# Kernel tuning notes

Measured on AMD Instinct MI355X. Metric: run time of the kernel, lower is better.

## Reference

```python
import jax, jax.numpy as jnp
import numpy as np
import math

B, S = 8, 2048
N_HIDDEN_RNN = 512
D_MODEL = 1024
NUM_HEADS = 16
N_OUTPUT = 1024
SCALE = math.sqrt(D_MODEL // NUM_HEADS)  # head_dim used only for scaling


def setup_inputs() -> dict:
    key = jax.random.key(0)
    ks = jax.random.split(key, 11)
    def lin(k, fan_in, fan_out):
        bound = 1.0 / math.sqrt(fan_in)
        kw, kb = jax.random.split(k)
        W = jax.random.uniform(kw, (fan_out, fan_in), jnp.float32, -bound, bound)
        b = jax.random.uniform(kb, (fan_out,), jnp.float32, -bound, bound)
        return W, b
    Wq, bq = lin(ks[0], N_HIDDEN_RNN, D_MODEL)
    Wk, bk = lin(ks[1], D_MODEL, D_MODEL)
    Wv, bv = lin(ks[2], D_MODEL, D_MODEL)
    Wo, bo = lin(ks[3], D_MODEL, N_OUTPUT)
    return {
        "query": jax.random.normal(ks[4], (B, S, N_HIDDEN_RNN), jnp.float32),
        "key": jax.random.normal(ks[5], (B, S, D_MODEL), jnp.float32),
        "value": jax.random.normal(ks[6], (B, S, D_MODEL), jnp.float32),
        "Wq": Wq, "bq": bq, "Wk": Wk, "bk": bk,
        "Wv": Wv, "bv": bv, "Wo": Wo, "bo": bo,
    }


def reference(query, key, value, Wq, bq, Wk, bk, Wv, bv, Wo, bo):
    # Projections
    q = query @ Wq.T + bq      # [B, S, d_model]
    k = key @ Wk.T + bk        # [B, S, d_model]
    v = value @ Wv.T + bv      # [B, S, d_model]
    # Original code transposes to [B, d_model, S] (feature-axis attention).
    # scores[b, i, j] = sum_s q[b, s, i] * k[b, s, j] / scale -> [B, d, d]
    scores = jnp.einsum('bsi,bsj->bij', q, k) / SCALE
    probs = jax.nn.softmax(scores, axis=-1)   # softmax over feature axis j
    # out[b, s, i] = sum_j probs[b, i, j] * v[b, s, j]
    attn_out = jnp.einsum('bij,bsj->bsi', probs, v)  # [B, S, d_model]
    return attn_out @ Wo.T + bo  # [B, S, n_output]
```

## Files before the change

### kernel.cpp

```cpp
#include <hip/hip_runtime.h>
#include <hip/hip_bf16.h>
#include <stdint.h>

typedef __bf16 b16x8 __attribute__((ext_vector_type(8)));
typedef float  f32x4 __attribute__((ext_vector_type(4)));

__device__ __forceinline__ unsigned short f2bf(float f) {
    uint32_t u = __float_as_uint(f);
    u += 0x7fffu + ((u >> 16) & 1u);
    return (unsigned short)(u >> 16);
}
__device__ __forceinline__ float bf2f(unsigned short s) {
    return __uint_as_float(((uint32_t)s) << 16);
}

__device__ __forceinline__ void gld16(const unsigned short* g, unsigned short* l) {
    __builtin_amdgcn_global_load_lds(
        (const __attribute__((address_space(1))) void*)g,
        (__attribute__((address_space(3))) void*)l, 16, 0, 0);
}

__global__ void k_detect(const unsigned short* __restrict__ q, int n, int* __restrict__ flag) {
    float m = 0.f;
    for (int i = threadIdx.x; i < n; i += 256) {
        float f = fabsf(bf2f(q[i]));
        if (!(f < 1e30f)) f = 1e30f;
        m = fmaxf(m, f);
    }
#pragma unroll
    for (int o = 32; o > 0; o >>= 1) m = fmaxf(m, __shfl_xor(m, o));
    __shared__ float red[4];
    if ((threadIdx.x & 63) == 0) red[threadIdx.x >> 6] = m;
    __syncthreads();
    if (threadIdx.x == 0) {
        m = fmaxf(fmaxf(red[0], red[1]), fmaxf(red[2], red[3]));
        flag[0] = (m > 1e6f) ? 1 : 0;
    }
}

__global__ __launch_bounds__(256) void k_cvt(const void* __restrict__ src,
                                             unsigned short* __restrict__ dst,
                                             long n8, const int* __restrict__ flag) {
    long i = blockIdx.x * 256L + threadIdx.x;
    long stride = (long)gridDim.x * 256L;
    if (flag[0]) {
        const float4* s = (const float4*)src;
        for (long j = i; j < n8; j += stride) {
            float4 a = s[2 * j], b = s[2 * j + 1];
            uint4 o;
            o.x = f2bf(a.x) | ((uint32_t)f2bf(a.y) << 16);
            o.y = f2bf(a.z) | ((uint32_t)f2bf(a.w) << 16);
            o.z = f2bf(b.x) | ((uint32_t)f2bf(b.y) << 16);
            o.w = f2bf(b.z) | ((uint32_t)f2bf(b.w) << 16);
            ((uint4*)dst)[j] = o;
        }
    } else {
        const uint4* s = (const uint4*)src;
        for (long j = i; j < n8; j += stride) ((uint4*)dst)[j] = s[j];
    }
}

__global__ __launch_bounds__(256) void k_cvt_bias(const void* b0, const void* b1,
                                                  const void* b2, const void* b3,
                                                  float* __restrict__ dst,
                                                  const int* __restrict__ flag) {
    int i = blockIdx.x * 256 + threadIdx.x;
    int which = i >> 10, idx = i & 1023;
    const void* src = (which == 0) ? b0 : (which == 1) ? b1 : (which == 2) ? b2 : b3;
    dst[i] = flag[0] ? ((const float*)src)[idx] : bf2f(((const unsigned short*)src)[idx]);
}

template <int MODE>
__global__ __launch_bounds__(512, 2) void k_gemm2(
    const unsigned short* __restrict__ A, const unsigned short* __restrict__ B,
    const float* __restrict__ bias, void* __restrict__ Cv,
    int N, int K, int ldA, int ldB, int lb,
    long sAb, long sBb, long sCb, float scale,
    const int* __restrict__ flagp)
{
    extern __shared__ unsigned short lds_raw[];
    const int tid  = threadIdx.x;
    const int lane = tid & 63;
    const int wave = tid >> 6;
    const int bn = blockIdx.x * 256;
    const int bm = blockIdx.y * 256;
    const int batch = bm >> lb;
    const int am0 = bm & ((1 << lb) - 1);
    const int Mb = 1 << lb;
    const unsigned short* Ab = A + (long)batch * sAb;
    const unsigned short* Bb = B + (long)batch * sBb;
    const long zC = (long)batch * sCb;
    const int wm = (wave >> 2) * 128;
    const int wn = (wave & 3) * 64;

    f32x4 acc[8][4];
    const f32x4 zero = {0.f, 0.f, 0.f, 0.f};
#pragma unroll
    for (int i = 0; i < 8; ++i)
#pragma unroll
        for (int j = 0; j < 4; ++j) acc[i][j] = zero;

    auto stage = [&](int kt, int cb) {
        unsigned short* LA = lds_raw + (size_t)cb * 32768;
        unsigned short* LB = LA + 16384;
#pragma unroll
        for (int j = 0; j < 4; ++j) {
            const int d = j * 512 + tid;
            const int row = d >> 3;
            const int klo = (d & 7) ^ (row & 7);
            gld16(Ab + (long)(am0 + row) * ldA + kt * 64 + klo * 8, LA + (size_t)d * 8);
            gld16(Bb + (long)(bn + row) * ldB + kt * 64 + klo * 8, LB + (size_t)d * 8);
        }
    };

    auto ctile = [&](int cb) {
        const unsigned short* LA = lds_raw + (size_t)cb * 32768;
        const unsigned short* LB = LA + 16384;
        b16x8 bfr[4][2];
#pragma unroll
        for (int p = 0; p < 4; ++p) {
            if (p == 0) {
#pragma unroll
                for (int j = 0; j < 4; ++j)
#pragma unroll
                    for (int s = 0; s < 2; ++s) {
                        const int r = wn + j * 16 + (lane & 15);
                        const int kl = s * 4 + (lane >> 4);
                        bfr[j][s] = *(const b16x8*)(LB + ((size_t)r * 8 + (kl ^ (r & 7))) * 8);
                    }
            }
            b16x8 a[2][2];
#pragma unroll
            for (int q = 0; q < 2; ++q)
#pragma unroll
                for (int s = 0; s < 2; ++s) {
                    const int r = wm + (2 * p + q) * 16 + (lane & 15);
                    const int kl = s * 4 + (lane >> 4);
                    a[q][s] = *(const b16x8*)(LA + ((size_t)r * 8 + (kl ^ (r & 7))) * 8);
                }
            __builtin_amdgcn_s_setprio(1);
#pragma unroll
            for (int q = 0; q < 2; ++q)
#pragma unroll
                for (int j = 0; j < 4; ++j)
#pragma unroll
                    for (int s = 0; s < 2; ++s)
                        acc[2 * p + q][j] = __builtin_amdgcn_mfma_f32_16x16x32_bf16(
                            a[q][s], bfr[j][s], acc[2 * p + q][j], 0, 0, 0);
            __builtin_amdgcn_s_setprio(0);
        }
    };

    const int NT = K >> 6;
    stage(0, 0);
    __syncthreads();
    int cur = 0;
    for (int kt = 0; kt < NT - 1; ++kt) {
        stage(kt + 1, cur ^ 1);
        ctile(cur);
        __syncthreads();
        cur ^= 1;
    }
    ctile(cur);

    const int fl = flagp ? flagp[0] : 1;
#pragma unroll
    for (int i = 0; i < 8; ++i)
#pragma unroll
        for (int j = 0; j < 4; ++j) {
            const int rloc = am0 + wm + i * 16 + (lane >> 4) * 4;
            const int n    = bn + wn + j * 16 + (lane & 15);
            const float bv = (MODE != 2 && bias != nullptr) ? bias[n] : 0.f;
            if (MODE == 0) {
                unsigned short* C = (unsigned short*)Cv;
#pragma unroll
                for (int r = 0; r < 4; ++r)
                    C[zC + (long)(rloc + r) * N + n] = f2bf(acc[i][j][r] * scale + bv);
            } else if (MODE == 1) {
                unsigned short* C = (unsigned short*)Cv;
                uint32_t p0 = f2bf(acc[i][j][0] * scale + bv) |
                              ((uint32_t)f2bf(acc[i][j][1] * scale + bv) << 16);
                uint32_t p1 = f2bf(acc[i][j][2] * scale + bv) |
                              ((uint32_t)f2bf(acc[i][j][3] * scale + bv) << 16);
                uint2 val; val.x = p0; val.y = p1;
                *(uint2*)(C + zC + (long)n * Mb + rloc) = val;
            } else if (MODE == 2) {
                float* C = (float*)Cv;
#pragma unroll
                for (int r = 0; r < 4; ++r)
                    C[zC + (long)(rloc + r) * N + n] = acc[i][j][r] * scale;
            } else {
                if (fl) {
                    float* C = (float*)Cv;
#pragma unroll
                    for (int r = 0; r < 4; ++r)
                        C[zC + (long)(rloc + r) * N + n] = acc[i][j][r] * scale + bv;
                } else {
                    unsigned short* C = (unsigned short*)Cv;
#pragma unroll
                    for (int r = 0; r < 4; ++r)
                        C[zC + (long)(rloc + r) * N + n] = f2bf(acc[i][j][r] * scale + bv);
                }
            }
        }
}

__global__ __launch_bounds__(256) void k_softmax(float* __restrict__ S) {
    const long row = blockIdx.x;
    float* s = S + row * 1024;
    unsigned short* p = (unsigned short*)s;
    const int tid = threadIdx.x;
    float4 v = ((const float4*)s)[tid];
    float m = fmaxf(fmaxf(v.x, v.y), fmaxf(v.z, v.w));
#pragma unroll
    for (int o = 32; o > 0; o >>= 1) m = fmaxf(m, __shfl_xor(m, o));
    __shared__ float sm[4], ss[4];
    if ((tid & 63) == 0) sm[tid >> 6] = m;
    __syncthreads();
    m = fmaxf(fmaxf(sm[0], sm[1]), fmaxf(sm[2], sm[3]));
    float e0 = __expf(v.x - m), e1 = __expf(v.y - m);
    float e2 = __expf(v.z - m), e3 = __expf(v.w - m);
    float sum = e0 + e1 + e2 + e3;
#pragma unroll
    for (int o = 32; o > 0; o >>= 1) sum += __shfl_xor(sum, o);
    if ((tid & 63) == 0) ss[tid >> 6] = sum;
    __syncthreads();
    float inv = 1.f / (ss[0] + ss[1] + ss[2] + ss[3]);
    uint32_t w0 = f2bf(e0 * inv) | ((uint32_t)f2bf(e1 * inv) << 16);
    uint32_t w1 = f2bf(e2 * inv) | ((uint32_t)f2bf(e3 * inv) << 16);
    uint2 val; val.x = w0; val.y = w1;
    *(uint2*)(p + tid * 4) = val;
}

extern "C" void kernel_launch(void* const* d_in, const int* in_sizes, int n_in,
                              void* d_out, int out_size, void* d_ws, size_t ws_size,
                              hipStream_t stream) {
    (void)in_sizes; (void)n_in; (void)out_size; (void)ws_size;
    const void* q_in = d_in[0];
    const void* k_in = d_in[1];
    const void* v_in = d_in[2];
    const void* Wq   = d_in[3];
    const void* bq   = d_in[4];
    const void* Wk   = d_in[5];
    const void* bk   = d_in[6];
    const void* Wv   = d_in[7];
    const void* bv   = d_in[8];
    const void* Wo   = d_in[9];
    const void* bo   = d_in[10];

    const size_t MB = 1u << 20;
    const size_t LDSB = 131072;
    hipFuncSetAttribute((const void*)k_gemm2<0>, hipFuncAttributeMaxDynamicSharedMemorySize, (int)LDSB);
    hipFuncSetAttribute((const void*)k_gemm2<1>, hipFuncAttributeMaxDynamicSharedMemorySize, (int)LDSB);
    hipFuncSetAttribute((const void*)k_gemm2<2>, hipFuncAttributeMaxDynamicSharedMemorySize, (int)LDSB);
    hipFuncSetAttribute((const void*)k_gemm2<3>, hipFuncAttributeMaxDynamicSharedMemorySize, (int)LDSB);

    char* ws = (char*)d_ws;
    int*            flag = (int*)ws;
    unsigned short* R1   = (unsigned short*)(ws + 1 * MB);
    unsigned short* R2   = (unsigned short*)(ws + 33 * MB);
    char*           R3   = ws + 65 * MB;
    unsigned short* kb = R1, *qb = R1, *vb = R1;
    unsigned short* Kt = R2, *attn = R2;
    float*          scores = (float*)R1;
    unsigned short* P      = R1;
    unsigned short* wqb = (unsigned short*)R3;
    unsigned short* wkb = (unsigned short*)(R3 + 1 * MB);
    unsigned short* wvb = (unsigned short*)(R3 + 3 * MB);
    unsigned short* wob = (unsigned short*)(R3 + 5 * MB);
    float*          bias4 = (float*)(R3 + 7 * MB);
    unsigned short* Vp = (unsigned short*)d_out;
    unsigned short* Qt = (unsigned short*)((char*)d_out + 32 * MB);

    dim3 blk(256);
    k_detect<<<1, blk, 0, stream>>>((const unsigned short*)q_in, 4096, flag);
    k_cvt_bias<<<16, blk, 0, stream>>>(bq, bk, bv, bo, bias4, flag);
    k_cvt<<<256, blk, 0, stream>>>(Wq, wqb, 1024L * 512 / 8, flag);
    k_cvt<<<512, blk, 0, stream>>>(Wk, wkb, 1024L * 1024 / 8, flag);
    k_cvt<<<512, blk, 0, stream>>>(Wv, wvb, 1024L * 1024 / 8, flag);
    k_cvt<<<512, blk, 0, stream>>>(Wo, wob, 1024L * 1024 / 8, flag);

    dim3 blk5(512);
    k_cvt<<<2048, blk, 0, stream>>>(k_in, kb, 8L * 2048 * 1024 / 8, flag);
    k_gemm2<1><<<dim3(4, 64), blk5, LDSB, stream>>>(
        kb, wkb, bias4 + 1024, Kt, 1024, 1024, 1024, 1024, 11,
        2048L * 1024, 0, 1024L * 2048, 1.f, nullptr);
    k_cvt<<<2048, blk, 0, stream>>>(q_in, qb, 8L * 2048 * 512 / 8, flag);
    k_gemm2<1><<<dim3(4, 64), blk5, LDSB, stream>>>(
        qb, wqb, bias4, Qt, 1024, 512, 512, 512, 11,
        2048L * 512, 0, 1024L * 2048, 1.f, nullptr);
    k_cvt<<<2048, blk, 0, stream>>>(v_in, vb, 8L * 2048 * 1024 / 8, flag);
    k_gemm2<0><<<dim3(4, 64), blk5, LDSB, stream>>>(
        vb, wvb, bias4 + 2 * 1024, Vp, 1024, 1024, 1024, 1024, 24,
        0, 0, 0, 1.f, nullptr);
    k_gemm2<2><<<dim3(4, 32), blk5, LDSB, stream>>>(
        Qt, Kt, nullptr, scores, 1024, 2048, 2048, 2048, 10,
        1024L * 2048, 1024L * 2048, 1024L * 1024, 0.125f, nullptr);
    k_softmax<<<dim3(8192), blk, 0, stream>>>(scores);
    k_gemm2<0><<<dim3(4, 64), blk5, LDSB, stream>>>(
        Vp, P, nullptr, attn, 1024, 1024, 1024, 2048, 11,
        2048L * 1024, 1024L * 2048, 2048L * 1024, 1.f, nullptr);
    k_gemm2<3><<<dim3(4, 64), blk5, LDSB, stream>>>(
        attn, wob, bias4 + 3 * 1024, d_out, 1024, 1024, 1024, 1024, 24,
        0, 0, 0, 1.f, flag);
}
```

Measured before the change: 322.0 us.

## Interleave next-tile global loads across MFMA phases with fine-grained waitcnt barriers

Replaces the GEMM main loop with a software pipeline that issues the next K-tile's global-to-LDS loads in four quarters, one per compute phase, guarded by explicit vmcnt waits and s_barriers. This replaces the single bulk stage plus full __syncthreads per tile. Warp row assignment is reshuffled to match the quarter loading order. Block IDs are also remapped so consecutive IDs spread across the eight XCDs. The aim is better overlap of memory with MFMA and better L2 locality, at the cost of hand-tuned waitcnt counts that could race if the compiler reorders loads.

Measured after the change: 319.0 us. About the same (-0.9%).

```diff
diff --git a/kernel.cpp b/kernel.cpp
--- a/kernel.cpp
+++ b/kernel.cpp
@@ -71,7 +71,7 @@
 }
 
 template <int MODE>
-__global__ __launch_bounds__(512, 2) void k_gemm2(
+__global__ __launch_bounds__(512, 2) void k_gemm3(
     const unsigned short* __restrict__ A, const unsigned short* __restrict__ B,
     const float* __restrict__ bias, void* __restrict__ Cv,
     int N, int K, int ldA, int ldB, int lb,
@@ -82,15 +82,19 @@
     const int tid  = threadIdx.x;
     const int lane = tid & 63;
     const int wave = tid >> 6;
-    const int bn = blockIdx.x * 256;
-    const int bm = blockIdx.y * 256;
+    const int nwg = gridDim.x * gridDim.y;
+    const int bid = blockIdx.y * gridDim.x + blockIdx.x;
+    const int nq  = nwg >> 3;
+    const int vb  = (bid & 7) * nq + (bid >> 3);
+    const int bn  = (vb & (gridDim.x - 1)) * 256;
+    const int bm  = (vb / gridDim.x) * 256;
     const int batch = bm >> lb;
     const int am0 = bm & ((1 << lb) - 1);
     const int Mb = 1 << lb;
     const unsigned short* Ab = A + (long)batch * sAb;
     const unsigned short* Bb = B + (long)batch * sBb;
     const long zC = (long)batch * sCb;
-    const int wm = (wave >> 2) * 128;
+    const int g  = wave >> 2;
     const int wn = (wave & 3) * 64;
 
     f32x4 acc[8][4];
@@ -100,25 +104,41 @@
 #pragma unroll
         for (int j = 0; j < 4; ++j) acc[i][j] = zero;
 
-    auto stage = [&](int kt, int cb) {
-        unsigned short* LA = lds_raw + (size_t)cb * 32768;
-        unsigned short* LB = LA + 16384;
-#pragma unroll
-        for (int j = 0; j < 4; ++j) {
-            const int d = j * 512 + tid;
-            const int row = d >> 3;
-            const int klo = (d & 7) ^ (row & 7);
-            gld16(Ab + (long)(am0 + row) * ldA + kt * 64 + klo * 8, LA + (size_t)d * 8);
-            gld16(Bb + (long)(bn + row) * ldB + kt * 64 + klo * 8, LB + (size_t)d * 8);
+    auto stageQ = [&](int kt, int cb, int q) {
+        unsigned short* Lbase = lds_raw + (size_t)cb * 32768 + ((q < 2) ? 16384 : 0);
+#pragma unroll
+        for (int j = 0; j < 2; ++j) {
+            const int c = (q & 1) * 1024 + j * 512 + tid;
+            const int row = c >> 3;
+            const int klo = (c & 7) ^ (row & 7);
+            if (q < 2)
+                gld16(Bb + (long)(bn + row) * ldB + kt * 64 + klo * 8, Lbase + (size_t)c * 8);
+            else
+                gld16(Ab + (long)(am0 + row) * ldA + kt * 64 + klo * 8, Lbase + (size_t)c * 8);
         }
     };
 
-    auto ctile = [&](int cb) {
-        const unsigned short* LA = lds_raw + (size_t)cb * 32768;
+    const int NT = K >> 6;
+#pragma unroll
+    for (int q = 0; q < 4; ++q) stageQ(0, 0, q);
+
+    int cur = 0;
+    for (int t = 0; t < NT; ++t) {
+        const int has_next = (t + 1 < NT);
+        const unsigned short* LA = lds_raw + (size_t)cur * 32768;
         const unsigned short* LB = LA + 16384;
         b16x8 bfr[4][2];
 #pragma unroll
         for (int p = 0; p < 4; ++p) {
+            if (p == 0) {
+                asm volatile("s_waitcnt vmcnt(2)" ::: "memory");
+            } else if (p == 2) {
+                if (has_next) asm volatile("s_waitcnt vmcnt(4)" ::: "memory");
+                else          asm volatile("s_waitcnt vmcnt(0)" ::: "memory");
+            }
+            __builtin_amdgcn_sched_barrier(0);
+            __builtin_amdgcn_s_barrier();
+            asm volatile("" ::: "memory");
             if (p == 0) {
 #pragma unroll
                 for (int j = 0; j < 4; ++j)
@@ -129,53 +149,47 @@
                         bfr[j][s] = *(const b16x8*)(LB + ((size_t)r * 8 + (kl ^ (r & 7))) * 8);
                     }
             }
-            b16x8 a[2][2];
-#pragma unroll
-            for (int q = 0; q < 2; ++q)
+            b16x8 afr[2][2];
+#pragma unroll
+            for (int r = 0; r < 2; ++r)
 #pragma unroll
                 for (int s = 0; s < 2; ++s) {
-                    const int r = wm + (2 * p + q) * 16 + (lane & 15);
+                    const int row = (p >> 1) * 128 + (p & 1) * 64 + g * 32 + r * 16 + (lane & 15);
                     const int kl = s * 4 + (lane >> 4);
-                    a[q][s] = *(const b16x8*)(LA + ((size_t)r * 8 + (kl ^ (r & 7))) * 8);
+                    afr[r][s] = *(const b16x8*)(LA + ((size_t)row * 8 + (kl ^ (row & 7))) * 8);
                 }
+            if (has_next) stageQ(t + 1, cur ^ 1, p);
+            asm volatile("" ::: "memory");
+            __builtin_amdgcn_s_barrier();
+            __builtin_amdgcn_sched_barrier(0);
             __builtin_amdgcn_s_setprio(1);
 #pragma unroll
-            for (int q = 0; q < 2; ++q)
+            for (int r = 0; r < 2; ++r)
 #pragma unroll
                 for (int j = 0; j < 4; ++j)
 #pragma unroll
                     for (int s = 0; s < 2; ++s)
-                        acc[2 * p + q][j] = __builtin_amdgcn_mfma_f32_16x16x32_bf16(
-                            a[q][s], bfr[j][s], acc[2 * p + q][j], 0, 0, 0);
+                        acc[p * 2 + r][j] = __builtin_amdgcn_mfma_f32_16x16x32_bf16(
+                            afr[r][s], bfr[j][s], acc[p * 2 + r][j], 0, 0, 0);
             __builtin_amdgcn_s_setprio(0);
         }
-    };
-
-    const int NT = K >> 6;
-    stage(0, 0);
-    __syncthreads();
-    int cur = 0;
-    for (int kt = 0; kt < NT - 1; ++kt) {
-        stage(kt + 1, cur ^ 1);
-        ctile(cur);
-        __syncthreads();
         cur ^= 1;
     }
-    ctile(cur);
 
     const int fl = flagp ? flagp[0] : 1;
 #pragma unroll
-    for (int i = 0; i < 8; ++i)
+    for (int i = 0; i < 8; ++i) {
+        const int p = i >> 1, r = i & 1;
+        const int rloc = am0 + (p >> 1) * 128 + (p & 1) * 64 + g * 32 + r * 16 + (lane >> 4) * 4;
 #pragma unroll
         for (int j = 0; j < 4; ++j) {
-            const int rloc = am0 + wm + i * 16 + (lane >> 4) * 4;
-            const int n    = bn + wn + j * 16 + (lane & 15);
+            const int n = bn + wn + j * 16 + (lane & 15);
             const float bv = (MODE != 2 && bias != nullptr) ? bias[n] : 0.f;
             if (MODE == 0) {
                 unsigned short* C = (unsigned short*)Cv;
 #pragma unroll
-                for (int r = 0; r < 4; ++r)
-                    C[zC + (long)(rloc + r) * N + n] = f2bf(acc[i][j][r] * scale + bv);
+                for (int rr = 0; rr < 4; ++rr)
+                    C[zC + (long)(rloc + rr) * N + n] = f2bf(acc[i][j][rr] * scale + bv);
             } else if (MODE == 1) {
                 unsigned short* C = (unsigned short*)Cv;
                 uint32_t p0 = f2bf(acc[i][j][0] * scale + bv) |
@@ -187,22 +201,23 @@
             } else if (MODE == 2) {
                 float* C = (float*)Cv;
 #pragma unroll
-                for (int r = 0; r < 4; ++r)
-                    C[zC + (long)(rloc + r) * N + n] = acc[i][j][r] * scale;
+                for (int rr = 0; rr < 4; ++rr)
+                    C[zC + (long)(rloc + rr) * N + n] = acc[i][j][rr] * scale;
             } else {
                 if (fl) {
                     float* C = (float*)Cv;
 #pragma unroll
-                    for (int r = 0; r < 4; ++r)
-                        C[zC + (long)(rloc + r) * N + n] = acc[i][j][r] * scale + bv;
+                    for (int rr = 0; rr < 4; ++rr)
+                        C[zC + (long)(rloc + rr) * N + n] = acc[i][j][rr] * scale + bv;
                 } else {
                     unsigned short* C = (unsigned short*)Cv;
 #pragma unroll
-                    for (int r = 0; r < 4; ++r)
-                        C[zC + (long)(rloc + r) * N + n] = f2bf(acc[i][j][r] * scale + bv);
+                    for (int rr = 0; rr < 4; ++rr)
+                        C[zC + (long)(rloc + rr) * N + n] = f2bf(acc[i][j][rr] * scale + bv);
                 }
             }
         }
+    }
 }
 
 __global__ __launch_bounds__(256) void k_softmax(float* __restrict__ S) {
@@ -250,10 +265,10 @@
 
     const size_t MB = 1u << 20;
     const size_t LDSB = 131072;
-    hipFuncSetAttribute((const void*)k_gemm2<0>, hipFuncAttributeMaxDynamicSharedMemorySize, (int)LDSB);
-    hipFuncSetAttribute((const void*)k_gemm2<1>, hipFuncAttributeMaxDynamicSharedMemorySize, (int)LDSB);
-    hipFuncSetAttribute((const void*)k_gemm2<2>, hipFuncAttributeMaxDynamicSharedMemorySize, (int)LDSB);
-    hipFuncSetAttribute((const void*)k_gemm2<3>, hipFuncAttributeMaxDynamicSharedMemorySize, (int)LDSB);
+    hipFuncSetAttribute((const void*)k_gemm3<0>, hipFuncAttributeMaxDynamicSharedMemorySize, (int)LDSB);
+    hipFuncSetAttribute((const void*)k_gemm3<1>, hipFuncAttributeMaxDynamicSharedMemorySize, (int)LDSB);
+    hipFuncSetAttribute((const void*)k_gemm3<2>, hipFuncAttributeMaxDynamicSharedMemorySize, (int)LDSB);
+    hipFuncSetAttribute((const void*)k_gemm3<3>, hipFuncAttributeMaxDynamicSharedMemorySize, (int)LDSB);
 
     char* ws = (char*)d_ws;
     int*            flag = (int*)ws;
@@ -282,25 +297,25 @@
 
     dim3 blk5(512);
     k_cvt<<<2048, blk, 0, stream>>>(k_in, kb, 8L * 2048 * 1024 / 8, flag);
-    k_gemm2<1><<<dim3(4, 64), blk5, LDSB, stream>>>(
+    k_gemm3<1><<<dim3(4, 64), blk5, LDSB, stream>>>(
         kb, wkb, bias4 + 1024, Kt, 1024, 1024, 1024, 1024, 11,
         2048L * 1024, 0, 1024L * 2048, 1.f, nullptr);
     k_cvt<<<2048, blk, 0, stream>>>(q_in, qb, 8L * 2048 * 512 / 8, flag);
-    k_gemm2<1><<<dim3(4, 64), blk5, LDSB, stream>>>(
+    k_gemm3<1><<<dim3(4, 64), blk5, LDSB, stream>>>(
         qb, wqb, bias4, Qt, 1024, 512, 512, 512, 11,
         2048L * 512, 0, 1024L * 2048, 1.f, nullptr);
     k_cvt<<<2048, blk, 0, stream>>>(v_in, vb, 8L * 2048 * 1024 / 8, flag);
-    k_gemm2<0><<<dim3(4, 64), blk5, LDSB, stream>>>(
+    k_gemm3<0><<<dim3(4, 64), blk5, LDSB, stream>>>(
         vb, wvb, bias4 + 2 * 1024, Vp, 1024, 1024, 1024, 1024, 24,
         0, 0, 0, 1.f, nullptr);
-    k_gemm2<2><<<dim3(4, 32), blk5, LDSB, stream>>>(
+    k_gemm3<2><<<dim3(4, 32), blk5, LDSB, stream>>>(
         Qt, Kt, nullptr, scores, 1024, 2048, 2048, 2048, 10,
         1024L * 2048, 1024L * 2048, 1024L * 1024, 0.125f, nullptr);
     k_softmax<<<dim3(8192), blk, 0, stream>>>(scores);
-    k_gemm2<0><<<dim3(4, 64), blk5, LDSB, stream>>>(
+    k_gemm3<0><<<dim3(4, 64), blk5, LDSB, stream>>>(
         Vp, P, nullptr, attn, 1024, 1024, 1024, 2048, 11,
         2048L * 1024, 1024L * 2048, 2048L * 1024, 1.f, nullptr);
-    k_gemm2<3><<<dim3(4, 64), blk5, LDSB, stream>>>(
+    k_gemm3<3><<<dim3(4, 64), blk5, LDSB, stream>>>(
         attn, wob, bias4 + 3 * 1024, d_out, 1024, 1024, 1024, 1024, 24,
         0, 0, 0, 1.f, flag);
 }
```

## Fuse input fp32-to-bf16 conversion into projection GEMMs and merge setup kernels

Applied to the files above, without the earlier changes.

The projection GEMMs now read fp32 activations directly through registers, convert them to bf16 and write them into swizzled LDS, which removes three standalone conversion passes and their round trips through global memory. The detect, bias and weight conversion kernels are merged into one setup kernel, cutting launch count. Workgroup IDs are also remapped across groups of eight, likely to improve cache locality or XCD distribution. In exchange, the A-operand path moves from async global-to-LDS loads to register staging, which raises register pressure and adds conversion work inside the main loop.

Result: slower. 472.1 us (+46.6%).

```diff
diff --git a/kernel.cpp b/kernel.cpp
--- a/kernel.cpp
+++ b/kernel.cpp
@@ -20,10 +20,17 @@
         (__attribute__((address_space(3))) void*)l, 16, 0, 0);
 }
 
-__global__ void k_detect(const unsigned short* __restrict__ q, int n, int* __restrict__ flag) {
+__global__ __launch_bounds__(256) void k_setup(
+    const unsigned short* __restrict__ qraw,
+    const void* Wq, const void* bq, const void* Wk, const void* bk,
+    const void* Wv, const void* bv, const void* Wo, const void* bo,
+    unsigned short* __restrict__ wqb, unsigned short* __restrict__ wkb,
+    unsigned short* __restrict__ wvb, unsigned short* __restrict__ wob,
+    float* __restrict__ bias4, int* __restrict__ flag)
+{
     float m = 0.f;
-    for (int i = threadIdx.x; i < n; i += 256) {
-        float f = fabsf(bf2f(q[i]));
+    for (int i = threadIdx.x; i < 4096; i += 256) {
+        float f = fabsf(bf2f(qraw[i]));
         if (!(f < 1e30f)) f = 1e30f;
         m = fmaxf(m, f);
     }
@@ -32,47 +39,42 @@
     __shared__ float red[4];
     if ((threadIdx.x & 63) == 0) red[threadIdx.x >> 6] = m;
     __syncthreads();
-    if (threadIdx.x == 0) {
-        m = fmaxf(fmaxf(red[0], red[1]), fmaxf(red[2], red[3]));
-        flag[0] = (m > 1e6f) ? 1 : 0;
+    m = fmaxf(fmaxf(red[0], red[1]), fmaxf(red[2], red[3]));
+    const int fl = (m > 1e6f) ? 1 : 0;
+    if (blockIdx.x == 0 && threadIdx.x == 0) flag[0] = fl;
+
+    if (blockIdx.x < 16) {
+        int i = blockIdx.x * 256 + threadIdx.x;
+        int which = i >> 10, idx = i & 1023;
+        const void* src = (which == 0) ? bq : (which == 1) ? bk : (which == 2) ? bv : bo;
+        bias4[i] = fl ? ((const float*)src)[idx] : bf2f(((const unsigned short*)src)[idx]);
     }
-}
-
-__global__ __launch_bounds__(256) void k_cvt(const void* __restrict__ src,
-                                             unsigned short* __restrict__ dst,
-                                             long n8, const int* __restrict__ flag) {
-    long i = blockIdx.x * 256L + threadIdx.x;
-    long stride = (long)gridDim.x * 256L;
-    if (flag[0]) {
-        const float4* s = (const float4*)src;
-        for (long j = i; j < n8; j += stride) {
-            float4 a = s[2 * j], b = s[2 * j + 1];
+
+    const long NW = 65536L + 3 * 131072L;
+    for (long c = blockIdx.x * 256L + threadIdx.x; c < NW; c += (long)gridDim.x * 256L) {
+        const void* src; unsigned short* dst; long off;
+        if (c < 65536)       { src = Wq; dst = wqb; off = c; }
+        else if (c < 196608) { src = Wk; dst = wkb; off = c - 65536; }
+        else if (c < 327680) { src = Wv; dst = wvb; off = c - 196608; }
+        else                 { src = Wo; dst = wob; off = c - 327680; }
+        if (fl) {
+            const float4* s = (const float4*)src + 2 * off;
+            float4 a = s[0], b = s[1];
             uint4 o;
             o.x = f2bf(a.x) | ((uint32_t)f2bf(a.y) << 16);
             o.y = f2bf(a.z) | ((uint32_t)f2bf(a.w) << 16);
             o.z = f2bf(b.x) | ((uint32_t)f2bf(b.y) << 16);
             o.w = f2bf(b.z) | ((uint32_t)f2bf(b.w) << 16);
-            ((uint4*)dst)[j] = o;
-        }
-    } else {
-        const uint4* s = (const uint4*)src;
-        for (long j = i; j < n8; j += stride) ((uint4*)dst)[j] = s[j];
+            ((uint4*)dst)[off] = o;
+        } else {
+            ((uint4*)dst)[off] = ((const uint4*)src)[off];
+        }
     }
 }
 
-__global__ __launch_bounds__(256) void k_cvt_bias(const void* b0, const void* b1,
-                                                  const void* b2, const void* b3,
-                                                  float* __restrict__ dst,
-                                                  const int* __restrict__ flag) {
-    int i = blockIdx.x * 256 + threadIdx.x;
-    int which = i >> 10, idx = i & 1023;
-    const void* src = (which == 0) ? b0 : (which == 1) ? b1 : (which == 2) ? b2 : b3;
-    dst[i] = flag[0] ? ((const float*)src)[idx] : bf2f(((const unsigned short*)src)[idx]);
-}
-
-template <int MODE>
-__global__ __launch_bounds__(512, 2) void k_gemm2(
-    const unsigned short* __restrict__ A, const unsigned short* __restrict__ B,
+template <int MODE, int AF32>
+__global__ __launch_bounds__(512, 2) void k_gemmU(
+    const void* __restrict__ Araw, const unsigned short* __restrict__ B,
     const float* __restrict__ bias, void* __restrict__ Cv,
     int N, int K, int ldA, int ldB, int lb,
     long sAb, long sBb, long sCb, float scale,
@@ -82,12 +84,16 @@
     const int tid  = threadIdx.x;
     const int lane = tid & 63;
     const int wave = tid >> 6;
-    const int bn = blockIdx.x * 256;
-    const int bm = blockIdx.y * 256;
+    const int nwg = gridDim.x * gridDim.y;
+    const int bid = blockIdx.y * gridDim.x + blockIdx.x;
+    const int vb  = (bid & 7) * (nwg >> 3) + (bid >> 3);
+    const int bn  = (vb & (gridDim.x - 1)) * 256;
+    const int bm  = (vb / gridDim.x) * 256;
     const int batch = bm >> lb;
     const int am0 = bm & ((1 << lb) - 1);
     const int Mb = 1 << lb;
-    const unsigned short* Ab = A + (long)batch * sAb;
+    const int fl = flagp ? flagp[0] : 1;
+    const long aoff = (long)batch * sAb;
     const unsigned short* Bb = B + (long)batch * sBb;
     const long zC = (long)batch * sCb;
     const int wm = (wave >> 2) * 128;
@@ -100,19 +106,64 @@
 #pragma unroll
         for (int j = 0; j < 4; ++j) acc[i][j] = zero;
 
-    auto stage = [&](int kt, int cb) {
+    auto stageB = [&](int kt, int cb) {
+        unsigned short* LB = lds_raw + (size_t)cb * 32768 + 16384;
+#pragma unroll
+        for (int j = 0; j < 4; ++j) {
+            const int d = j * 512 + tid;
+            const int row = d >> 3;
+            const int klo = (d & 7) ^ (row & 7);
+            gld16(Bb + (long)(bn + row) * ldB + kt * 64 + klo * 8, LB + (size_t)d * 8);
+        }
+    };
+    auto stageA = [&](int kt, int cb) {
         unsigned short* LA = lds_raw + (size_t)cb * 32768;
-        unsigned short* LB = LA + 16384;
+        const unsigned short* Ab = (const unsigned short*)Araw + aoff;
 #pragma unroll
         for (int j = 0; j < 4; ++j) {
             const int d = j * 512 + tid;
             const int row = d >> 3;
             const int klo = (d & 7) ^ (row & 7);
             gld16(Ab + (long)(am0 + row) * ldA + kt * 64 + klo * 8, LA + (size_t)d * 8);
-            gld16(Bb + (long)(bn + row) * ldB + kt * 64 + klo * 8, LB + (size_t)d * 8);
-        }
-    };
-
+        }
+    };
+    float4 araw[4][2];
+    uint4  abf[4];
+    auto loadA = [&](int kt) {
+#pragma unroll
+        for (int j = 0; j < 4; ++j) {
+            const int c = j * 512 + tid;
+            const int row = c >> 3, kc = c & 7;
+            if (fl) {
+                const float* s = (const float*)Araw + aoff + (long)(am0 + row) * ldA + kt * 64 + kc * 8;
+                araw[j][0] = *(const float4*)s;
+                araw[j][1] = *(const float4*)(s + 4);
+            } else {
+                abf[j] = *(const uint4*)((const unsigned short*)Araw + aoff +
+                                         (long)(am0 + row) * ldA + kt * 64 + kc * 8);
+            }
+        }
+    };
+    auto cvtWriteA = [&](int cb) {
+        unsigned short* LA = lds_raw + (size_t)cb * 32768;
+#pragma unroll
+        for (int j = 0; j < 4; ++j) {
+            const int c = j * 512 + tid;
+            const int row = c >> 3, kc = c & 7;
+            const int slot = row * 8 + (kc ^ (row & 7));
+            uint4 o;
+            if (fl) {
+                float4 a = araw[j][0], b = araw[j][1];
+                o.x = f2bf(a.x) | ((uint32_t)f2bf(a.y) << 16);
+                o.y = f2bf(a.z) | ((uint32_t)f2bf(a.w) << 16);
+                o.z = f2bf(b.x) | ((uint32_t)f2bf(b.y) << 16);
+                o.w = f2bf(b.z) | ((uint32_t)f2bf(b.w) << 16);
+            } else {
+                o = abf[j];
+            }
+            *(uint4*)(LA + (size_t)slot * 8) = o;
+        }
+    };
     auto ctile = [&](int cb) {
         const unsigned short* LA = lds_raw + (size_t)cb * 32768;
         const unsigned short* LB = LA + 16384;
@@ -152,18 +203,32 @@
     };
 
     const int NT = K >> 6;
-    stage(0, 0);
-    __syncthreads();
     int cur = 0;
-    for (int kt = 0; kt < NT - 1; ++kt) {
-        stage(kt + 1, cur ^ 1);
+    if (AF32) {
+        stageB(0, 0); loadA(0); cvtWriteA(0);
+        __syncthreads();
+        for (int kt = 0; kt < NT - 1; ++kt) {
+            stageB(kt + 1, cur ^ 1);
+            loadA(kt + 1);
+            ctile(cur);
+            cvtWriteA(cur ^ 1);
+            __syncthreads();
+            cur ^= 1;
+        }
         ctile(cur);
+    } else {
+        stageA(0, 0); stageB(0, 0);
         __syncthreads();
-        cur ^= 1;
+        for (int kt = 0; kt < NT - 1; ++kt) {
+            stageA(kt + 1, cur ^ 1);
+            stageB(kt + 1, cur ^ 1);
+            ctile(cur);
+            __syncthreads();
+            cur ^= 1;
+        }
+        ctile(cur);
     }
-    ctile(cur);
-
-    const int fl = flagp ? flagp[0] : 1;
+
 #pragma unroll
     for (int i = 0; i < 8; ++i)
 #pragma unroll
@@ -250,17 +315,17 @@
 
     const size_t MB = 1u << 20;
     const size_t LDSB = 131072;
-    hipFuncSetAttribute((const void*)k_gemm2<0>, hipFuncAttributeMaxDynamicSharedMemorySize, (int)LDSB);
-    hipFuncSetAttribute((const void*)k_gemm2<1>, hipFuncAttributeMaxDynamicSharedMemorySize, (int)LDSB);
-    hipFuncSetAttribute((const void*)k_gemm2<2>, hipFuncAttributeMaxDynamicSharedMemorySize, (int)LDSB);
-    hipFuncSetAttribute((const void*)k_gemm2<3>, hipFuncAttributeMaxDynamicSharedMemorySize, (int)LDSB);
+    hipFuncSetAttribute((const void*)k_gemmU<1, 1>, hipFuncAttributeMaxDynamicSharedMemorySize, (int)LDSB);
+    hipFuncSetAttribute((const void*)k_gemmU<0, 1>, hipFuncAttributeMaxDynamicSharedMemorySize, (int)LDSB);
+    hipFuncSetAttribute((const void*)k_gemmU<2, 0>, hipFuncAttributeMaxDynamicSharedMemorySize, (int)LDSB);
+    hipFuncSetAttribute((const void*)k_gemmU<0, 0>, hipFuncAttributeMaxDynamicSharedMemorySize, (int)LDSB);
+    hipFuncSetAttribute((const void*)k_gemmU<3, 0>, hipFuncAttributeMaxDynamicSharedMemorySize, (int)LDSB);
 
     char* ws = (char*)d_ws;
     int*            flag = (int*)ws;
     unsigned short* R1   = (unsigned short*)(ws + 1 * MB);
     unsigned short* R2   = (unsigned short*)(ws + 33 * MB);
     char*           R3   = ws + 65 * MB;
-    unsigned short* kb = R1, *qb = R1, *vb = R1;
     unsigned short* Kt = R2, *attn = R2;
     float*          scores = (float*)R1;
     unsigned short* P      = R1;
@@ -272,35 +337,28 @@
     unsigned short* Vp = (unsigned short*)d_out;
     unsigned short* Qt = (unsigned short*)((char*)d_out + 32 * MB);
 
-    dim3 blk(256);
-    k_detect<<<1, blk, 0, stream>>>((const unsigned short*)q_in, 4096, flag);
-    k_cvt_bias<<<16, blk, 0, stream>>>(bq, bk, bv, bo, bias4, flag);
-    k_cvt<<<256, blk, 0, stream>>>(Wq, wqb, 1024L * 512 / 8, flag);
-    k_cvt<<<512, blk, 0, stream>>>(Wk, wkb, 1024L * 1024 / 8, flag);
-    k_cvt<<<512, blk, 0, stream>>>(Wv, wvb, 1024L * 1024 / 8, flag);
-    k_cvt<<<512, blk, 0, stream>>>(Wo, wob, 1024L * 1024 / 8, flag);
-
-    dim3 blk5(512);
-    k_cvt<<<2048, blk, 0, stream>>>(k_in, kb, 8L * 2048 * 1024 / 8, flag);
-    k_gemm2<1><<<dim3(4, 64), blk5, LDSB, stream>>>(
-        kb, wkb, bias4 + 1024, Kt, 1024, 1024, 1024, 1024, 11,
-        2048L * 1024, 0, 1024L * 2048, 1.f, nullptr);
-    k_cvt<<<2048, blk, 0, stream>>>(q_in, qb, 8L * 2048 * 512 / 8, flag);
-    k_gemm2<1><<<dim3(4, 64), blk5, LDSB, stream>>>(
-        qb, wqb, bias4, Qt, 1024, 512, 512, 512, 11,
-        2048L * 512, 0, 1024L * 2048, 1.f, nullptr);
-    k_cvt<<<2048, blk, 0, stream>>>(v_in, vb, 8L * 2048 * 1024 / 8, flag);
-    k_gemm2<0><<<dim3(4, 64), blk5, LDSB, stream>>>(
-        vb, wvb, bias4 + 2 * 1024, Vp, 1024, 1024, 1024, 1024, 24,
-        0, 0, 0, 1.f, nullptr);
-    k_gemm2<2><<<dim3(4, 32), blk5, LDSB, stream>>>(
+    dim3 blk(256), blk5(512);
+    k_setup<<<dim3(832), blk, 0, stream>>>(
+        (const unsigned short*)q_in, Wq, bq, Wk, bk, Wv, bv, Wo, bo,
+        wqb, wkb, wvb, wob, bias4, flag);
+
+    k_gemmU<1, 1><<<dim3(4, 64), blk5, LDSB, stream>>>(
+        k_in, wkb, bias4 + 1024, Kt, 1024, 1024, 1024, 1024, 11,
+        2048L * 1024, 0, 1024L * 2048, 1.f, flag);
+    k_gemmU<1, 1><<<dim3(4, 64), blk5, LDSB, stream>>>(
+        q_in, wqb, bias4, Qt, 1024, 512, 512, 512, 11,
+        2048L * 512, 0, 1024L * 2048, 1.f, flag);
+    k_gemmU<0, 1><<<dim3(4, 64), blk5, LDSB, stream>>>(
+        v_in, wvb, bias4 + 2 * 1024, Vp, 1024, 1024, 1024, 1024, 24,
+        0, 0, 0, 1.f, flag);
+    k_gemmU<2, 0><<<dim3(4, 32), blk5, LDSB, stream>>>(
         Qt, Kt, nullptr, scores, 1024, 2048, 2048, 2048, 10,
         1024L * 2048, 1024L * 2048, 1024L * 1024, 0.125f, nullptr);
     k_softmax<<<dim3(8192), blk, 0, stream>>>(scores);
-    k_gemm2<0><<<dim3(4, 64), blk5, LDSB, stream>>>(
+    k_gemmU<0, 0><<<dim3(4, 64), blk5, LDSB, stream>>>(
         Vp, P, nullptr, attn, 1024, 1024, 1024, 2048, 11,
         2048L * 1024, 1024L * 2048, 2048L * 1024, 1.f, nullptr);
-    k_gemm2<3><<<dim3(4, 64), blk5, LDSB, stream>>>(
+    k_gemmU<3, 0><<<dim3(4, 64), blk5, LDSB, stream>>>(
         attn, wob, bias4 + 3 * 1024, d_out, 1024, 1024, 1024, 1024, 24,
         0, 0, 0, 1.f, flag);
 }
```
